# Kernel tuning notes

Hardware: AMD Instinct MI355X
Metric: run time of the kernel (lower is better)

## Reference

```python
import jax, jax.numpy as jnp
import numpy as np

# int64 needed: the torch module hashes with int64 primes (2654435761 > 2**31)
jax.config.update("jax_enable_x64", True)

NUM_LEVELS = 16
BASE_RES = 16
MAX_RES = 2048
LOG2_HASHMAP = 19
FEATURE_DIM = 2
HASHMAP_SIZE = 2 ** LOG2_HASHMAP
N_POINTS = 1_048_576

_growth = np.exp((np.log(MAX_RES) - np.log(BASE_RES)) / (NUM_LEVELS - 1))
RESOLUTIONS = [min(int(BASE_RES * _growth ** l), MAX_RES) for l in range(NUM_LEVELS)]
PRIMES = np.array([1, 2654435761, 805459861], dtype=np.int64)
# corner order matches torch triple loop: index c = i*4 + j*2 + k -> offset [i, j, k]
OFFSETS = np.array([[i, j, k] for i in range(2) for j in range(2) for k in range(2)],
                   dtype=np.int64)  # (8, 3)


def setup_inputs() -> dict:
    key = jax.random.key(0)
    k1, k2 = jax.random.split(key)
    positions = jax.random.uniform(k1, (N_POINTS, 3), dtype=jnp.float32) * 2.0 - 1.0  # in [-1, 1]
    hash_table = jax.random.normal(k2, (HASHMAP_SIZE, FEATURE_DIM), dtype=jnp.float32) * 1e-4
    return {"positions": positions, "hash_table": hash_table}


def _encode(positions, hash_table):
    p = (positions + 1.0) * 0.5  # map [-1,1] -> [0,1]
    primes = jnp.asarray(PRIMES)
    offs = jnp.asarray(OFFSETS)           # (8, 3) int64
    offs_f = offs.astype(p.dtype)         # (8, 3)
    feats = []
    for res in RESOLUTIONS:
        sp = p * (res - 1)                # (N, 3)
        gp = jnp.floor(sp)
        w = sp - gp                       # fractional weights (N, 3)
        corners = gp.astype(jnp.int64)[:, None, :] + offs[None]   # (N, 8, 3)
        corners = jnp.clip(corners, 0, res - 1)
        h = (corners[..., 0] * primes[0]) ^ (corners[..., 1] * primes[1]) ^ (corners[..., 2] * primes[2])
        idx = h % HASHMAP_SIZE            # (N, 8)
        cf = hash_table[idx]              # gather: (N, 8, F)
        # trilinear weights: prod over dims of (w if offset bit else 1-w)
        wcomp = offs_f[None] * w[:, None, :] + (1.0 - offs_f[None]) * (1.0 - w[:, None, :])  # (N,8,3)
        tw = wcomp[..., 0] * wcomp[..., 1] * wcomp[..., 2]        # (N, 8)
        feats.append(jnp.einsum('nc,ncf->nf', tw, cf))            # (N, F)
    return jnp.concatenate(feats, axis=-1)  # (N, NUM_LEVELS * F)


def reference(positions, hash_table):
    return _encode(positions, hash_table)
```

## Files before the change

kernel.cpp:

```cpp
#include <hip/hip_runtime.h>
#include <cstdint>

#define P2 2654435761u
#define P3 805459861u
#define HMASK 524287u
#define NBUCK 32768

typedef float nfloat4 __attribute__((ext_vector_type(4)));
typedef float nfloat2 __attribute__((ext_vector_type(2)));

__constant__ int RES[16] = {16, 22, 30, 42, 58, 80, 111, 153,
                            212, 294, 406, 561, 776, 1072, 1482, 2048};

__device__ __forceinline__ int bucket_of(float px, float py, float pz) {
    int bx = min(31, max(0, (int)((px + 1.0f) * 16.0f)));
    int by = min(31, max(0, (int)((py + 1.0f) * 16.0f)));
    int bz = min(31, max(0, (int)((pz + 1.0f) * 16.0f)));
    return (bx * 32 + by) * 32 + bz;
}

__global__ __launch_bounds__(256) void zero_counts(int* c) {
    int i = blockIdx.x * 256 + threadIdx.x;
    if (i < NBUCK) c[i] = 0;
}

__global__ __launch_bounds__(256) void count_kernel(
    const float* __restrict__ pos, int* __restrict__ counts, int n) {
    int i = blockIdx.x * 256 + threadIdx.x;
    if (i >= n) return;
    atomicAdd(&counts[bucket_of(pos[3*i], pos[3*i+1], pos[3*i+2])], 1);
}

__global__ __launch_bounds__(1024) void scan_kernel(int* counts) {
    __shared__ int part[1024];
    int t = threadIdx.x;
    int base = t * 32;
    int s = 0;
    #pragma unroll
    for (int j = 0; j < 32; ++j) s += counts[base + j];
    part[t] = s;
    __syncthreads();
    int orig = s;
    for (int off = 1; off < 1024; off <<= 1) {
        int v = (t >= off) ? part[t - off] : 0;
        __syncthreads();
        part[t] += v;
        __syncthreads();
    }
    int run = part[t] - orig;
    for (int j = 0; j < 32; ++j) {
        int c = counts[base + j];
        counts[base + j] = run;
        run += c;
    }
}

__global__ __launch_bounds__(256) void scatter_kernel(
    const float* __restrict__ pos, int* __restrict__ counts,
    int* __restrict__ perm, int n) {
    int i = blockIdx.x * 256 + threadIdx.x;
    if (i >= n) return;
    int b = bucket_of(pos[3*i], pos[3*i+1], pos[3*i+2]);
    int slot = atomicAdd(&counts[b], 1);
    perm[slot] = i;
}

__global__ __launch_bounds__(256) void hash_enc_sorted(
    const float* __restrict__ pos, const float2* __restrict__ tbl,
    float2* __restrict__ out, const int* __restrict__ perm,
    int n, int usePerm)
{
    const float4* __restrict__ tbl4 = (const float4*)tbl;

    __shared__ int   sidx[64];
    __shared__ float sx[64], sy[64], sz[64];
    __shared__ float2 sout[64][17];

    const int tid = threadIdx.x;
    const int base = blockIdx.x * 64;

    if (tid < 64) {
        int gi = base + tid;
        int pi = 0;
        if (gi < n) pi = usePerm ? perm[gi] : gi;
        sidx[tid] = pi;
        float px = pos[3*pi+0], py = pos[3*pi+1], pz = pos[3*pi+2];
        sx[tid] = (px + 1.0f) * 0.5f;
        sy[tid] = (py + 1.0f) * 0.5f;
        sz[tid] = (pz + 1.0f) * 0.5f;
    }
    __syncthreads();

    const int wave = tid >> 6, lane = tid & 63;
    const float x = sx[lane], y = sy[lane], z = sz[lane];

    #pragma unroll
    for (int s = 0; s < 4; ++s) {
        const int l = wave + 4 * s;
        const int rm1 = RES[l] - 1;
        const float rf = (float)rm1;

        float sxf = x * rf, syf = y * rf, szf = z * rf;
        float fx = floorf(sxf), fy = floorf(syf), fz = floorf(szf);
        float wx = sxf - fx, wy = syf - fy, wz = szf - fz;
        int x0 = (int)fx, y0 = (int)fy, z0 = (int)fz;
        int x0c = min(max(x0, 0), rm1), x1c = min(max(x0 + 1, 0), rm1);
        int y0c = min(max(y0, 0), rm1), y1c = min(max(y0 + 1, 0), rm1);
        int z0c = min(max(z0, 0), rm1), z1c = min(max(z0 + 1, 0), rm1);

        uint32_t hy0 = (uint32_t)y0c * P2, hy1 = (uint32_t)y1c * P2;
        uint32_t hz0 = (uint32_t)z0c * P3, hz1 = (uint32_t)z1c * P3;
        uint32_t m00 = hy0 ^ hz0, m01 = hy0 ^ hz1;
        uint32_t m10 = hy1 ^ hz0, m11 = hy1 ^ hz1;

        uint32_t hx0 = (uint32_t)x0c;
        uint32_t j000 = (hx0 ^ m00) & HMASK;
        uint32_t j001 = (hx0 ^ m01) & HMASK;
        uint32_t j010 = (hx0 ^ m10) & HMASK;
        uint32_t j011 = (hx0 ^ m11) & HMASK;

        float4 q00 = tbl4[j000 >> 1];
        float4 q01 = tbl4[j001 >> 1];
        float4 q10 = tbl4[j010 >> 1];
        float4 q11 = tbl4[j011 >> 1];

        bool b00 = (j000 & 1), b01 = (j001 & 1);
        bool b10 = (j010 & 1), b11 = (j011 & 1);
        float2 c000 = b00 ? make_float2(q00.z, q00.w) : make_float2(q00.x, q00.y);
        float2 c100 = b00 ? make_float2(q00.x, q00.y) : make_float2(q00.z, q00.w);
        float2 c001 = b01 ? make_float2(q01.z, q01.w) : make_float2(q01.x, q01.y);
        float2 c101 = b01 ? make_float2(q01.x, q01.y) : make_float2(q01.z, q01.w);
        float2 c010 = b10 ? make_float2(q10.z, q10.w) : make_float2(q10.x, q10.y);
        float2 c110 = b10 ? make_float2(q10.x, q10.y) : make_float2(q10.z, q10.w);
        float2 c011 = b11 ? make_float2(q11.z, q11.w) : make_float2(q11.x, q11.y);
        float2 c111 = b11 ? make_float2(q11.x, q11.y) : make_float2(q11.z, q11.w);

        if (x0c & 1) {
            uint32_t hx1 = (uint32_t)x1c;
            c100 = tbl[(hx1 ^ m00) & HMASK];
            c101 = tbl[(hx1 ^ m01) & HMASK];
            c110 = tbl[(hx1 ^ m10) & HMASK];
            c111 = tbl[(hx1 ^ m11) & HMASK];
        }

        float ux = 1.0f - wx, uy = 1.0f - wy, uz = 1.0f - wz;
        float w00 = ux * uy, w01 = ux * wy, w10 = wx * uy, w11 = wx * wy;
        float f0, f1;
        f0  = (w00 * uz) * c000.x; f1  = (w00 * uz) * c000.y;
        f0 += (w00 * wz) * c001.x; f1 += (w00 * wz) * c001.y;
        f0 += (w01 * uz) * c010.x; f1 += (w01 * uz) * c010.y;
        f0 += (w01 * wz) * c011.x; f1 += (w01 * wz) * c011.y;
        f0 += (w10 * uz) * c100.x; f1 += (w10 * uz) * c100.y;
        f0 += (w10 * wz) * c101.x; f1 += (w10 * wz) * c101.y;
        f0 += (w11 * uz) * c110.x; f1 += (w11 * uz) * c110.y;
        f0 += (w11 * wz) * c111.x; f1 += (w11 * wz) * c111.y;

        sout[lane][l] = make_float2(f0, f1);
    }
    __syncthreads();

    int q = tid >> 2, part = tid & 3;
    if (base + q < n) {
        int oi = sidx[q] * 16 + part * 4;
        float2 a = sout[q][part*4+0], b = sout[q][part*4+1];
        float2 c = sout[q][part*4+2], d = sout[q][part*4+3];
        nfloat4 v0; v0.x = a.x; v0.y = a.y; v0.z = b.x; v0.w = b.y;
        nfloat4 v1; v1.x = c.x; v1.y = c.y; v1.z = d.x; v1.w = d.y;
        __builtin_nontemporal_store(v0, (nfloat4*)&out[oi]);
        __builtin_nontemporal_store(v1, (nfloat4*)&out[oi + 2]);
    }
}

extern "C" void kernel_launch(void* const* d_in, const int* in_sizes, int n_in,
                              void* d_out, int out_size, void* d_ws, size_t ws_size,
                              hipStream_t stream) {
    const float* pos = (const float*)d_in[0];
    const float2* tbl = (const float2*)d_in[1];
    float2* out = (float2*)d_out;
    int n = in_sizes[0] / 3;

    size_t need = (size_t)NBUCK * 4 + (size_t)n * 4;
    int usePerm = (ws_size >= need) ? 1 : 0;
    int* counts = (int*)d_ws;
    int* perm = counts + NBUCK;

    if (usePerm) {
        zero_counts<<<dim3((NBUCK + 255) / 256), dim3(256), 0, stream>>>(counts);
        count_kernel<<<dim3((n + 255) / 256), dim3(256), 0, stream>>>(pos, counts, n);
        scan_kernel<<<dim3(1), dim3(1024), 0, stream>>>(counts);
        scatter_kernel<<<dim3((n + 255) / 256), dim3(256), 0, stream>>>(pos, counts, perm, n);
    }

    hash_enc_sorted<<<dim3((n + 63) / 64), dim3(256), 0, stream>>>(
        pos, tbl, out, perm, n, usePerm);
}
```

Measured before the change: 521.5 us.

## Replace counting sort with fixed-capacity spatial buckets and overflow list

Drops the separate count, scan and scatter kernels. A single placement kernel atomically appends each point into a fixed 128-slot superbucket, with an overflow array for full buckets. The encoder launches two 64-point blocks per superbucket plus overflow blocks, masks inactive lanes, and writes output through a wider 8-thread store pattern. This removes a pass and the serial scan, but leaves many blocks partly filled, since each bucket holds about 64 points on average, so lane utilisation in the gather kernel drops.

```diff
diff --git a/kernel.cpp b/kernel.cpp
--- a/kernel.cpp
+++ b/kernel.cpp
@@ -4,87 +4,86 @@
 #define P2 2654435761u
 #define P3 805459861u
 #define HMASK 524287u
-#define NBUCK 32768
+
+#define NSB 16384
+#define CAP 128
+#define OVF_CAP 65536
+#define OVF_BLOCKS 1024
 
 typedef float nfloat4 __attribute__((ext_vector_type(4)));
-typedef float nfloat2 __attribute__((ext_vector_type(2)));
 
 __constant__ int RES[16] = {16, 22, 30, 42, 58, 80, 111, 153,
                             212, 294, 406, 561, 776, 1072, 1482, 2048};
 
-__device__ __forceinline__ int bucket_of(float px, float py, float pz) {
+__global__ __launch_bounds__(256) void zero_counts(int* c) {
+    int i = blockIdx.x * 256 + threadIdx.x;
+    if (i < NSB + 1) c[i] = 0;
+}
+
+__global__ __launch_bounds__(256) void place_kernel(
+    const float* __restrict__ pos, int* __restrict__ counts,
+    int* __restrict__ novf, int* __restrict__ perm,
+    int* __restrict__ ovfperm, int n)
+{
+    int i = blockIdx.x * 256 + threadIdx.x;
+    if (i >= n) return;
+    float px = pos[3*i], py = pos[3*i+1], pz = pos[3*i+2];
     int bx = min(31, max(0, (int)((px + 1.0f) * 16.0f)));
     int by = min(31, max(0, (int)((py + 1.0f) * 16.0f)));
     int bz = min(31, max(0, (int)((pz + 1.0f) * 16.0f)));
-    return (bx * 32 + by) * 32 + bz;
-}
-
-__global__ __launch_bounds__(256) void zero_counts(int* c) {
-    int i = blockIdx.x * 256 + threadIdx.x;
-    if (i < NBUCK) c[i] = 0;
-}
-
-__global__ __launch_bounds__(256) void count_kernel(
-    const float* __restrict__ pos, int* __restrict__ counts, int n) {
-    int i = blockIdx.x * 256 + threadIdx.x;
-    if (i >= n) return;
-    atomicAdd(&counts[bucket_of(pos[3*i], pos[3*i+1], pos[3*i+2])], 1);
-}
-
-__global__ __launch_bounds__(1024) void scan_kernel(int* counts) {
-    __shared__ int part[1024];
-    int t = threadIdx.x;
-    int base = t * 32;
-    int s = 0;
-    #pragma unroll
-    for (int j = 0; j < 32; ++j) s += counts[base + j];
-    part[t] = s;
-    __syncthreads();
-    int orig = s;
-    for (int off = 1; off < 1024; off <<= 1) {
-        int v = (t >= off) ? part[t - off] : 0;
-        __syncthreads();
-        part[t] += v;
-        __syncthreads();
-    }
-    int run = part[t] - orig;
-    for (int j = 0; j < 32; ++j) {
-        int c = counts[base + j];
-        counts[base + j] = run;
-        run += c;
-    }
-}
-
-__global__ __launch_bounds__(256) void scatter_kernel(
-    const float* __restrict__ pos, int* __restrict__ counts,
-    int* __restrict__ perm, int n) {
-    int i = blockIdx.x * 256 + threadIdx.x;
-    if (i >= n) return;
-    int b = bucket_of(pos[3*i], pos[3*i+1], pos[3*i+2]);
-    int slot = atomicAdd(&counts[b], 1);
-    perm[slot] = i;
+    int sb = (bx * 32 + by) * 16 + (bz >> 1);
+    int slot = atomicAdd(&counts[sb], 1);
+    if (slot < CAP) {
+        perm[sb * CAP + slot] = i;
+    } else {
+        int o = atomicAdd(novf, 1);
+        if (o < OVF_CAP) ovfperm[o] = i;
+    }
 }
 
 __global__ __launch_bounds__(256) void hash_enc_sorted(
     const float* __restrict__ pos, const float2* __restrict__ tbl,
     float2* __restrict__ out, const int* __restrict__ perm,
-    int n, int usePerm)
+    const int* __restrict__ ovfperm, const int* __restrict__ counts,
+    const int* __restrict__ novf, int n, int usePerm)
 {
     const float4* __restrict__ tbl4 = (const float4*)tbl;
 
-    __shared__ int   sidx[64];
-    __shared__ float sx[64], sy[64], sz[64];
+    __shared__ int    sidx[64];
+    __shared__ float  sx[64], sy[64], sz[64];
     __shared__ float2 sout[64][17];
 
     const int tid = threadIdx.x;
-    const int base = blockIdx.x * 64;
+    const int bid = blockIdx.x;
+
+    int nActive, sb = 0, chunk = 0, obase = 0;
+    if (usePerm) {
+        if (bid < 2 * NSB) {
+            sb = bid >> 1; chunk = bid & 1;
+            int cnt = min(counts[sb], CAP);
+            nActive = min(max(cnt - chunk * 64, 0), 64);
+        } else {
+            obase = (bid - 2 * NSB) * 64;
+            int nov = min(*novf, OVF_CAP);
+            nActive = min(max(nov - obase, 0), 64);
+        }
+    } else {
+        nActive = min(n - bid * 64, 64);
+    }
+    if (nActive <= 0) return;
 
     if (tid < 64) {
-        int gi = base + tid;
-        int pi = 0;
-        if (gi < n) pi = usePerm ? perm[gi] : gi;
+        int pi = -1;
+        if (tid < nActive) {
+            if (usePerm)
+                pi = (bid < 2 * NSB) ? perm[sb * CAP + chunk * 64 + tid]
+                                     : ovfperm[obase + tid];
+            else
+                pi = bid * 64 + tid;
+        }
         sidx[tid] = pi;
-        float px = pos[3*pi+0], py = pos[3*pi+1], pz = pos[3*pi+2];
+        float px = 0.f, py = 0.f, pz = 0.f;
+        if (pi >= 0) { px = pos[3*pi]; py = pos[3*pi+1]; pz = pos[3*pi+2]; }
         sx[tid] = (px + 1.0f) * 0.5f;
         sy[tid] = (py + 1.0f) * 0.5f;
         sz[tid] = (pz + 1.0f) * 0.5f;
@@ -92,82 +91,87 @@
     __syncthreads();
 
     const int wave = tid >> 6, lane = tid & 63;
+    const bool act = (lane < nActive);
     const float x = sx[lane], y = sy[lane], z = sz[lane];
 
     #pragma unroll
     for (int s = 0; s < 4; ++s) {
         const int l = wave + 4 * s;
-        const int rm1 = RES[l] - 1;
-        const float rf = (float)rm1;
-
-        float sxf = x * rf, syf = y * rf, szf = z * rf;
-        float fx = floorf(sxf), fy = floorf(syf), fz = floorf(szf);
-        float wx = sxf - fx, wy = syf - fy, wz = szf - fz;
-        int x0 = (int)fx, y0 = (int)fy, z0 = (int)fz;
-        int x0c = min(max(x0, 0), rm1), x1c = min(max(x0 + 1, 0), rm1);
-        int y0c = min(max(y0, 0), rm1), y1c = min(max(y0 + 1, 0), rm1);
-        int z0c = min(max(z0, 0), rm1), z1c = min(max(z0 + 1, 0), rm1);
-
-        uint32_t hy0 = (uint32_t)y0c * P2, hy1 = (uint32_t)y1c * P2;
-        uint32_t hz0 = (uint32_t)z0c * P3, hz1 = (uint32_t)z1c * P3;
-        uint32_t m00 = hy0 ^ hz0, m01 = hy0 ^ hz1;
-        uint32_t m10 = hy1 ^ hz0, m11 = hy1 ^ hz1;
-
-        uint32_t hx0 = (uint32_t)x0c;
-        uint32_t j000 = (hx0 ^ m00) & HMASK;
-        uint32_t j001 = (hx0 ^ m01) & HMASK;
-        uint32_t j010 = (hx0 ^ m10) & HMASK;
-        uint32_t j011 = (hx0 ^ m11) & HMASK;
-
-        float4 q00 = tbl4[j000 >> 1];
-        float4 q01 = tbl4[j001 >> 1];
-        float4 q10 = tbl4[j010 >> 1];
-        float4 q11 = tbl4[j011 >> 1];
-
-        bool b00 = (j000 & 1), b01 = (j001 & 1);
-        bool b10 = (j010 & 1), b11 = (j011 & 1);
-        float2 c000 = b00 ? make_float2(q00.z, q00.w) : make_float2(q00.x, q00.y);
-        float2 c100 = b00 ? make_float2(q00.x, q00.y) : make_float2(q00.z, q00.w);
-        float2 c001 = b01 ? make_float2(q01.z, q01.w) : make_float2(q01.x, q01.y);
-        float2 c101 = b01 ? make_float2(q01.x, q01.y) : make_float2(q01.z, q01.w);
-        float2 c010 = b10 ? make_float2(q10.z, q10.w) : make_float2(q10.x, q10.y);
-        float2 c110 = b10 ? make_float2(q10.x, q10.y) : make_float2(q10.z, q10.w);
-        float2 c011 = b11 ? make_float2(q11.z, q11.w) : make_float2(q11.x, q11.y);
-        float2 c111 = b11 ? make_float2(q11.x, q11.y) : make_float2(q11.z, q11.w);
-
-        if (x0c & 1) {
-            uint32_t hx1 = (uint32_t)x1c;
-            c100 = tbl[(hx1 ^ m00) & HMASK];
-            c101 = tbl[(hx1 ^ m01) & HMASK];
-            c110 = tbl[(hx1 ^ m10) & HMASK];
-            c111 = tbl[(hx1 ^ m11) & HMASK];
-        }
-
-        float ux = 1.0f - wx, uy = 1.0f - wy, uz = 1.0f - wz;
-        float w00 = ux * uy, w01 = ux * wy, w10 = wx * uy, w11 = wx * wy;
-        float f0, f1;
-        f0  = (w00 * uz) * c000.x; f1  = (w00 * uz) * c000.y;
-        f0 += (w00 * wz) * c001.x; f1 += (w00 * wz) * c001.y;
-        f0 += (w01 * uz) * c010.x; f1 += (w01 * uz) * c010.y;
-        f0 += (w01 * wz) * c011.x; f1 += (w01 * wz) * c011.y;
-        f0 += (w10 * uz) * c100.x; f1 += (w10 * uz) * c100.y;
-        f0 += (w10 * wz) * c101.x; f1 += (w10 * wz) * c101.y;
-        f0 += (w11 * uz) * c110.x; f1 += (w11 * uz) * c110.y;
-        f0 += (w11 * wz) * c111.x; f1 += (w11 * wz) * c111.y;
-
-        sout[lane][l] = make_float2(f0, f1);
+        if (act) {
+            const int rm1 = RES[l] - 1;
+            const float rf = (float)rm1;
+
+            float sxf = x * rf, syf = y * rf, szf = z * rf;
+            float fx = floorf(sxf), fy = floorf(syf), fz = floorf(szf);
+            float wx = sxf - fx, wy = syf - fy, wz = szf - fz;
+            int x0 = (int)fx, y0 = (int)fy, z0 = (int)fz;
+            int x0c = min(max(x0, 0), rm1), x1c = min(max(x0 + 1, 0), rm1);
+            int y0c = min(max(y0, 0), rm1), y1c = min(max(y0 + 1, 0), rm1);
+            int z0c = min(max(z0, 0), rm1), z1c = min(max(z0 + 1, 0), rm1);
+
+            uint32_t hy0 = (uint32_t)y0c * P2, hy1 = (uint32_t)y1c * P2;
+            uint32_t hz0 = (uint32_t)z0c * P3, hz1 = (uint32_t)z1c * P3;
+            uint32_t m00 = hy0 ^ hz0, m01 = hy0 ^ hz1;
+            uint32_t m10 = hy1 ^ hz0, m11 = hy1 ^ hz1;
+
+            uint32_t hx0 = (uint32_t)x0c;
+            uint32_t j000 = (hx0 ^ m00) & HMASK;
+            uint32_t j001 = (hx0 ^ m01) & HMASK;
+            uint32_t j010 = (hx0 ^ m10) & HMASK;
+            uint32_t j011 = (hx0 ^ m11) & HMASK;
+
+            float4 q00 = tbl4[j000 >> 1];
+            float4 q01 = tbl4[j001 >> 1];
+            float4 q10 = tbl4[j010 >> 1];
+            float4 q11 = tbl4[j011 >> 1];
+
+            bool b00 = (j000 & 1), b01 = (j001 & 1);
+            bool b10 = (j010 & 1), b11 = (j011 & 1);
+            float2 c000 = b00 ? make_float2(q00.z, q00.w) : make_float2(q00.x, q00.y);
+            float2 c100 = b00 ? make_float2(q00.x, q00.y) : make_float2(q00.z, q00.w);
+            float2 c001 = b01 ? make_float2(q01.z, q01.w) : make_float2(q01.x, q01.y);
+            float2 c101 = b01 ? make_float2(q01.x, q01.y) : make_float2(q01.z, q01.w);
+            float2 c010 = b10 ? make_float2(q10.z, q10.w) : make_float2(q10.x, q10.y);
+            float2 c110 = b10 ? make_float2(q10.x, q10.y) : make_float2(q10.z, q10.w);
+            float2 c011 = b11 ? make_float2(q11.z, q11.w) : make_float2(q11.x, q11.y);
+            float2 c111 = b11 ? make_float2(q11.x, q11.y) : make_float2(q11.z, q11.w);
+
+            if (x0c & 1) {
+                uint32_t hx1 = (uint32_t)x1c;
+                c100 = tbl[(hx1 ^ m00) & HMASK];
+                c101 = tbl[(hx1 ^ m01) & HMASK];
+                c110 = tbl[(hx1 ^ m10) & HMASK];
+                c111 = tbl[(hx1 ^ m11) & HMASK];
+            }
+
+            float ux = 1.0f - wx, uy = 1.0f - wy, uz = 1.0f - wz;
+            float w00 = ux * uy, w01 = ux * wy, w10 = wx * uy, w11 = wx * wy;
+            float f0, f1;
+            f0  = (w00 * uz) * c000.x; f1  = (w00 * uz) * c000.y;
+            f0 += (w00 * wz) * c001.x; f1 += (w00 * wz) * c001.y;
+            f0 += (w01 * uz) * c010.x; f1 += (w01 * uz) * c010.y;
+            f0 += (w01 * wz) * c011.x; f1 += (w01 * wz) * c011.y;
+            f0 += (w10 * uz) * c100.x; f1 += (w10 * uz) * c100.y;
+            f0 += (w10 * wz) * c101.x; f1 += (w10 * wz) * c101.y;
+            f0 += (w11 * uz) * c110.x; f1 += (w11 * uz) * c110.y;
+            f0 += (w11 * wz) * c111.x; f1 += (w11 * wz) * c111.y;
+
+            sout[lane][l] = make_float2(f0, f1);
+        }
     }
     __syncthreads();
 
-    int q = tid >> 2, part = tid & 3;
-    if (base + q < n) {
-        int oi = sidx[q] * 16 + part * 4;
-        float2 a = sout[q][part*4+0], b = sout[q][part*4+1];
-        float2 c = sout[q][part*4+2], d = sout[q][part*4+3];
-        nfloat4 v0; v0.x = a.x; v0.y = a.y; v0.z = b.x; v0.w = b.y;
-        nfloat4 v1; v1.x = c.x; v1.y = c.y; v1.z = d.x; v1.w = d.y;
-        __builtin_nontemporal_store(v0, (nfloat4*)&out[oi]);
-        __builtin_nontemporal_store(v1, (nfloat4*)&out[oi + 2]);
+    #pragma unroll
+    for (int half = 0; half < 2; ++half) {
+        int q = half * 32 + (tid >> 3);
+        int part = tid & 7;
+        int pi = sidx[q];
+        if (pi >= 0) {
+            float2 a = sout[q][part * 2], b = sout[q][part * 2 + 1];
+            nfloat4 v; v.x = a.x; v.y = a.y; v.z = b.x; v.w = b.y;
+            __builtin_nontemporal_store(
+                v, (nfloat4*)(out + ((size_t)pi * 16 + part * 2)));
+        }
     }
 }
 
@@ -179,18 +183,20 @@
     float2* out = (float2*)d_out;
     int n = in_sizes[0] / 3;
 
-    size_t need = (size_t)NBUCK * 4 + (size_t)n * 4;
+    size_t need = (size_t)(NSB + 64 + OVF_CAP + (size_t)NSB * CAP) * 4;
     int usePerm = (ws_size >= need) ? 1 : 0;
-    int* counts = (int*)d_ws;
-    int* perm = counts + NBUCK;
+    int* counts  = (int*)d_ws;
+    int* novf    = counts + NSB;
+    int* ovfperm = novf + 64;
+    int* perm    = ovfperm + OVF_CAP;
 
     if (usePerm) {
-        zero_counts<<<dim3((NBUCK + 255) / 256), dim3(256), 0, stream>>>(counts);
-        count_kernel<<<dim3((n + 255) / 256), dim3(256), 0, stream>>>(pos, counts, n);
-        scan_kernel<<<dim3(1), dim3(1024), 0, stream>>>(counts);
-        scatter_kernel<<<dim3((n + 255) / 256), dim3(256), 0, stream>>>(pos, counts, perm, n);
-    }
-
-    hash_enc_sorted<<<dim3((n + 63) / 64), dim3(256), 0, stream>>>(
-        pos, tbl, out, perm, n, usePerm);
-}
+        zero_counts<<<dim3((NSB + 256) / 256), dim3(256), 0, stream>>>(counts);
+        place_kernel<<<dim3((n + 255) / 256), dim3(256), 0, stream>>>(
+            pos, counts, novf, perm, ovfperm, n);
+    }
+
+    unsigned grid = usePerm ? (2 * NSB + OVF_BLOCKS) : (unsigned)((n + 63) / 64);
+    hash_enc_sorted<<<dim3(grid), dim3(256), 0, stream>>>(
+        pos, tbl, out, perm, ovfperm, counts, novf, n, usePerm);
+}
```

Measured after the change: 662.8 us. 27.1% more time.
